# Kernel tuning notes

Measured on AMD Instinct MI355X. Metric: run time of the kernel, lower is better.

The kernel has to match this reference:

```python
import jax, jax.numpy as jnp
import numpy as np

N, IN_F, E, EDGE_F, H, C = 50000, 128, 800000, 32, 4, 32
NEG_SLOPE = 0.2
EPS = 1e-16


def setup_inputs() -> dict:
    key = jax.random.key(0)
    ks = jax.random.split(key, 10)
    s = lambda *sh: 1.0 / np.sqrt(sh[-1])
    return {
        "node_features": jax.random.normal(ks[0], (N, IN_F), jnp.float32),
        "edge_features": jax.random.normal(ks[1], (E, EDGE_F), jnp.float32),
        "edge_index": jax.random.randint(ks[2], (2, E), 0, N, jnp.int32),
        # GATConv params
        "W_gat": jax.random.normal(ks[3], (H * C, IN_F), jnp.float32) * s(IN_F),
        "att_src": jax.random.normal(ks[4], (H, C), jnp.float32) * s(C),
        "att_dst": jax.random.normal(ks[5], (H, C), jnp.float32) * s(C),
        "att_edge": jax.random.normal(ks[6], (H, C), jnp.float32) * s(C),
        "bias": jnp.zeros((H * C,), jnp.float32),
        # edge_linear and skip_connection weights
        "W_edge": jax.random.normal(ks[7], (H * C, EDGE_F), jnp.float32) * s(EDGE_F),
        "W_skip": jax.random.normal(ks[8], (H * C, IN_F), jnp.float32) * s(IN_F),
    }


def reference(node_features, edge_features, edge_index, W_gat, att_src, att_dst,
              att_edge, bias, W_edge, W_skip):
    src, dst = edge_index[0], edge_index[1]
    # edge_linear + view(-1, H, C)
    e_attr = (edge_features @ W_edge.T).reshape(E, H, C)
    # GATConv: per-head linear transform of nodes -> [N, H, C]
    x = (node_features @ W_gat.T).reshape(N, H, C)
    # attention logits: a_src.x_i + a_dst.x_j + a_edge.e  -> [E, H]
    a_src = jnp.einsum('nhc,hc->nh', x, att_src)
    a_dst = jnp.einsum('nhc,hc->nh', x, att_dst)
    a_edge = jnp.einsum('ehc,hc->eh', e_attr, att_edge)
    alpha = jax.nn.leaky_relu(a_src[src] + a_dst[dst] + a_edge, NEG_SLOPE)
    # segment softmax over incoming edges of each destination node
    m = jax.ops.segment_max(alpha, dst, num_segments=N)  # [N, H]
    m = jnp.where(jnp.isfinite(m), m, 0.0)
    ex = jnp.exp(alpha - m[dst])
    denom = jax.ops.segment_sum(ex, dst, num_segments=N)  # [N, H]
    attn = ex / (denom[dst] + EPS)  # [E, H]
    # message = alpha * x_src ; scatter-add to destination
    msg = x[src] * attn[:, :, None]  # [E, H, C]
    out = jax.ops.segment_sum(msg, dst, num_segments=N)  # [N, H, C]
    out = out.reshape(N, H * C) + bias  # concat=True
    # skip connection + ELU activation
    out = out + node_features @ W_skip.T
    return jax.nn.elu(out)
```

## Files before the change

### kernel.cpp

```cpp
#include <hip/hip_runtime.h>
#include <hip/hip_bf16.h>

constexpr int N_NODES = 50000;
constexpr int IN_F    = 128;
constexpr long E_EDGES = 800000;
constexpr int EDGE_F  = 32;
constexpr int H_HEADS = 4;
constexpr int C_CH    = 32;
constexpr int HC      = 128;
constexpr float NEG_SLOPE = 0.2f;
constexpr float EPS = 1e-16f;
constexpr int NB_SCAN = (N_NODES + 255) / 256;
constexpr int NB_HIST = (int)((E_EDGES + 255) / 256);
constexpr float SM_SHIFT = 12.0f;

typedef __attribute__((ext_vector_type(8))) short bf16x8;
typedef __attribute__((ext_vector_type(4))) float f32x4;

__device__ __forceinline__ unsigned short f2b(float f) {
    __hip_bfloat16 h = __float2bfloat16(f);
    return *reinterpret_cast<unsigned short*>(&h);
}
__device__ __forceinline__ float b2f_lo(unsigned v) { return __uint_as_float(v << 16); }
__device__ __forceinline__ float b2f_hi(unsigned v) { return __uint_as_float(v & 0xffff0000u); }

__global__ __launch_bounds__(256) void prep_kernel(
    const float* __restrict__ Wg, const float* __restrict__ Ws,
    unsigned short* __restrict__ wcat, const float* __restrict__ We,
    const float* __restrict__ att_edge, float* __restrict__ weff,
    const int* __restrict__ dst, int* __restrict__ counts,
    int* __restrict__ rank)
{
    const int b = blockIdx.x, t = threadIdx.x;
    if (b < 32) {
        int i = (b * 256 + t) * 4;
        const float* srcp = (i < 16384) ? (Wg + i) : (Ws + i - 16384);
        float4 v = *(const float4*)srcp;
        ushort4 o;
        o.x = f2b(v.x); o.y = f2b(v.y); o.z = f2b(v.z); o.w = f2b(v.w);
        *(ushort4*)&wcat[i] = o;
    } else if (b == 32) {
        if (t < 128) {
            int h = t >> 5, f = t & 31;
            float acc = 0.f;
#pragma unroll
            for (int c = 0; c < C_CH; ++c)
                acc = fmaf(We[(h * C_CH + c) * EDGE_F + f], att_edge[h * C_CH + c], acc);
            weff[t] = acc;
        }
    } else {
        long e = (long)(b - 33) * 256 + t;
        if (e < E_EDGES) rank[e] = atomicAdd(&counts[dst[e]], 1);
    }
}

__global__ __launch_bounds__(256) void mfma_gemm_kernel(
    const float* __restrict__ nf, const unsigned short* __restrict__ wcat,
    const float* __restrict__ bias, unsigned short* __restrict__ xb,
    float* __restrict__ out)
{
    const int t  = threadIdx.x;
    const int w  = t >> 6;
    const int l  = t & 63;
    const int lr = l & 15;
    const int lk = l >> 4;
    const int n0 = blockIdx.x * 64;

    bf16x8 bfr[4][4];
#pragma unroll
    for (int nfr = 0; nfr < 4; ++nfr)
#pragma unroll
        for (int ks = 0; ks < 4; ++ks)
            bfr[nfr][ks] = *(const bf16x8*)&wcat[(w * 64 + nfr * 16 + lr) * 128 + ks * 32 + lk * 8];

    f32x4 acc[4][4];
#pragma unroll
    for (int mf = 0; mf < 4; ++mf)
#pragma unroll
        for (int nfr = 0; nfr < 4; ++nfr)
            acc[mf][nfr] = (f32x4){0.f, 0.f, 0.f, 0.f};

#pragma unroll
    for (int ks = 0; ks < 4; ++ks) {
        bf16x8 afr[4];
#pragma unroll
        for (int mf = 0; mf < 4; ++mf) {
            int row = n0 + mf * 16 + lr;
            row = row < N_NODES ? row : N_NODES - 1;
            const float* ap = nf + (size_t)row * IN_F + ks * 32 + lk * 8;
            float4 a0 = *(const float4*)ap;
            float4 a1 = *(const float4*)(ap + 4);
            bf16x8 f;
            f[0] = (short)f2b(a0.x); f[1] = (short)f2b(a0.y);
            f[2] = (short)f2b(a0.z); f[3] = (short)f2b(a0.w);
            f[4] = (short)f2b(a1.x); f[5] = (short)f2b(a1.y);
            f[6] = (short)f2b(a1.z); f[7] = (short)f2b(a1.w);
            afr[mf] = f;
        }
#pragma unroll
        for (int mf = 0; mf < 4; ++mf)
#pragma unroll
            for (int nfr = 0; nfr < 4; ++nfr)
                acc[mf][nfr] = __builtin_amdgcn_mfma_f32_16x16x32_bf16(
                    afr[mf], bfr[nfr][ks], acc[mf][nfr], 0, 0, 0);
    }

#pragma unroll
    for (int nfr = 0; nfr < 4; ++nfr) {
        const int gc = w * 64 + nfr * 16 + lr;
        if (gc < HC) {
#pragma unroll
            for (int mf = 0; mf < 4; ++mf)
#pragma unroll
                for (int r = 0; r < 4; ++r) {
                    int m = n0 + mf * 16 + lk * 4 + r;
                    if (m < N_NODES) xb[(size_t)m * HC + gc] = f2b(acc[mf][nfr][r]);
                }
        } else {
            const float bv = bias[gc - HC];
#pragma unroll
            for (int mf = 0; mf < 4; ++mf)
#pragma unroll
                for (int r = 0; r < 4; ++r) {
                    int m = n0 + mf * 16 + lk * 4 + r;
                    if (m < N_NODES) out[(size_t)m * HC + gc - HC] = acc[mf][nfr][r] + bv;
                }
        }
    }
}

__global__ __launch_bounds__(256) void a_kernel(
    const unsigned int* __restrict__ xb32, const float* __restrict__ att_src,
    const float* __restrict__ att_dst, float* __restrict__ asrc,
    float* __restrict__ adst)
{
    const int wave = threadIdx.x >> 6, lane = threadIdx.x & 63;
    const int n = blockIdx.x * 4 + wave;
    if (n >= N_NODES) return;
    unsigned v = xb32[(size_t)n * 64 + lane];
    float x0 = b2f_lo(v), x1 = b2f_hi(v);
    float2 as = ((const float2*)att_src)[lane];
    float2 ad = ((const float2*)att_dst)[lane];
    float ps = x0 * as.x + x1 * as.y;
    float pd = x0 * ad.x + x1 * ad.y;
#pragma unroll
    for (int off = 1; off < 16; off <<= 1) {
        ps += __shfl_xor(ps, off);
        pd += __shfl_xor(pd, off);
    }
    if ((lane & 15) == 0) {
        asrc[(size_t)n * H_HEADS + (lane >> 4)] = ps;
        adst[(size_t)n * H_HEADS + (lane >> 4)] = pd;
    }
}

__global__ __launch_bounds__(256) void scan1_kernel(const int* __restrict__ counts,
                                                    int* __restrict__ row_ptr,
                                                    int* __restrict__ blocksum)
{
    __shared__ int s[256];
    int t = threadIdx.x;
    int i = blockIdx.x * 256 + t;
    int v = (i < N_NODES) ? counts[i] : 0;
    s[t] = v;
    __syncthreads();
#pragma unroll
    for (int off = 1; off < 256; off <<= 1) {
        int u = (t >= off) ? s[t - off] : 0;
        __syncthreads();
        s[t] += u;
        __syncthreads();
    }
    if (i < N_NODES) row_ptr[i] = s[t] - v;
    if (t == 255) blocksum[blockIdx.x] = s[255];
}

__global__ __launch_bounds__(256) void scan2_kernel(int* __restrict__ blocksum)
{
    __shared__ int s[256];
    int t = threadIdx.x;
    int v = (t < NB_SCAN) ? blocksum[t] : 0;
    s[t] = v;
    __syncthreads();
#pragma unroll
    for (int off = 1; off < 256; off <<= 1) {
        int u = (t >= off) ? s[t - off] : 0;
        __syncthreads();
        s[t] += u;
        __syncthreads();
    }
    blocksum[t] = s[t] - v;
}

__global__ __launch_bounds__(256) void scan3_kernel(int* __restrict__ row_ptr,
                                                    const int* __restrict__ blocksum)
{
    int i = blockIdx.x * 256 + threadIdx.x;
    if (i < N_NODES) row_ptr[i] = row_ptr[i] + blocksum[blockIdx.x];
    if (i == 0) row_ptr[N_NODES] = (int)E_EDGES;
}

__global__ __launch_bounds__(256) void edge_logits_kernel(
    const float* __restrict__ ef, const int* __restrict__ src,
    const int* __restrict__ dst, const float* __restrict__ weff,
    const float* __restrict__ asrc, const float* __restrict__ adst,
    const int* __restrict__ row_ptr, const int* __restrict__ rank,
    unsigned int* __restrict__ rec)
{
    __shared__ float ef_lds[64][36];
    __shared__ float wf[4][36];
    const int t = threadIdx.x;
    const long e0 = (long)blockIdx.x * 64;

#pragma unroll
    for (int j = 0; j < 2; ++j) {
        int i4 = t + j * 256;
        int el = i4 >> 3, f4 = i4 & 7;
        long e = e0 + el;
        float4 v = (e < E_EDGES) ? ((const float4*)ef)[e * 8 + f4]
                                 : make_float4(0.f, 0.f, 0.f, 0.f);
        ef_lds[el][f4 * 4 + 0] = v.x; ef_lds[el][f4 * 4 + 1] = v.y;
        ef_lds[el][f4 * 4 + 2] = v.z; ef_lds[el][f4 * 4 + 3] = v.w;
    }
    if (t < 128) wf[t >> 5][t & 31] = weff[t];
    __syncthreads();

    const int el = t >> 2, h = t & 3;
    const long e = e0 + el;
    if (e < E_EDGES) {
        float acc = 0.f;
#pragma unroll
        for (int f4 = 0; f4 < 8; ++f4) {
            float4 a = *(const float4*)&ef_lds[el][f4 * 4];
            float4 b = *(const float4*)&wf[h][f4 * 4];
            acc = fmaf(a.x, b.x, acc); acc = fmaf(a.y, b.y, acc);
            acc = fmaf(a.z, b.z, acc); acc = fmaf(a.w, b.w, acc);
        }
        int s = src[e], d = dst[e];
        float logit = asrc[(size_t)s * H_HEADS + h] + adst[(size_t)d * H_HEADS + h] + acc;
        float al = logit > 0.f ? logit : NEG_SLOPE * logit;
        int pos = row_ptr[d] + rank[e];
        unsigned w = (__float_as_uint(al) & 0xFFFFFF00u)
                   | ((unsigned)(s >> (8 * h)) & 0xFFu);
        rec[(size_t)pos * 4 + h] = w;
    }
}

__device__ __forceinline__ void accum8(float* acc, uint4 v, float e) {
    acc[0] = fmaf(b2f_lo(v.x), e, acc[0]);
    acc[1] = fmaf(b2f_hi(v.x), e, acc[1]);
    acc[2] = fmaf(b2f_lo(v.y), e, acc[2]);
    acc[3] = fmaf(b2f_hi(v.y), e, acc[3]);
    acc[4] = fmaf(b2f_lo(v.z), e, acc[4]);
    acc[5] = fmaf(b2f_hi(v.z), e, acc[5]);
    acc[6] = fmaf(b2f_lo(v.w), e, acc[6]);
    acc[7] = fmaf(b2f_hi(v.w), e, acc[7]);
}

__device__ __forceinline__ int rec_src(uint4 r) {
    return (int)((r.x & 0xFFu) | ((r.y & 0xFFu) << 8));
}
__device__ __forceinline__ float rec_alpha(uint4 r, int h) {
    unsigned w = h == 0 ? r.x : h == 1 ? r.y : h == 2 ? r.z : r.w;
    return __uint_as_float(w & 0xFFFFFF00u);
}

__global__ __launch_bounds__(256) void aggregate_kernel(
    const int* __restrict__ row_ptr, const uint4* __restrict__ rec4,
    const uint4* __restrict__ xb4, float* __restrict__ out)
{
    const int wave = threadIdx.x >> 6;
    const int lane = threadIdx.x & 63;
    const int d = blockIdx.x * 4 + wave;
    if (d >= N_NODES) return;
    const int beg = row_ptr[d], end = row_ptr[d + 1];
    const int q  = lane >> 4;
    const int cg = lane & 15;
    const int h  = cg >> 2;

    float acc[8] = {0.f, 0.f, 0.f, 0.f, 0.f, 0.f, 0.f, 0.f};
    float dsum = 0.f;

    int i = beg;
    for (; i + 8 <= end; i += 8) {
        int i0 = i + q, i1 = i + 4 + q;
        uint4 r0 = rec4[i0];
        uint4 r1 = rec4[i1];
        int s0 = rec_src(r0);
        int s1 = rec_src(r1);
        float a0 = rec_alpha(r0, h);
        float a1 = rec_alpha(r1, h);
        uint4 v0 = xb4[(size_t)s0 * 16 + cg];
        uint4 v1 = xb4[(size_t)s1 * 16 + cg];
        float e0 = __expf(a0 - SM_SHIFT);
        float e1 = __expf(a1 - SM_SHIFT);
        dsum += e0 + e1;
        accum8(acc, v0, e0);
        accum8(acc, v1, e1);
    }
    for (; i < end; i += 4) {
        int idx = i + q;
        bool val = idx < end;
        int ii = val ? idx : end - 1;
        uint4 r = rec4[ii];
        int s = rec_src(r);
        float a = rec_alpha(r, h);
        uint4 v = xb4[(size_t)s * 16 + cg];
        float e = val ? __expf(a - SM_SHIFT) : 0.f;
        dsum += e;
        accum8(acc, v, e);
    }

#pragma unroll
    for (int off = 16; off <= 32; off <<= 1) {
        dsum += __shfl_xor(dsum, off);
#pragma unroll
        for (int k = 0; k < 8; ++k) acc[k] += __shfl_xor(acc[k], off);
    }
    const float inv = 1.f / (dsum + EPS);

    if (q == 0) {
        float* op = out + (size_t)d * HC + cg * 8;
        float4 o0 = *(const float4*)op;
        float4 o1 = *(const float4*)(op + 4);
        o0.x += acc[0] * inv; o0.y += acc[1] * inv;
        o0.z += acc[2] * inv; o0.w += acc[3] * inv;
        o1.x += acc[4] * inv; o1.y += acc[5] * inv;
        o1.z += acc[6] * inv; o1.w += acc[7] * inv;
        o0.x = o0.x > 0.f ? o0.x : expf(o0.x) - 1.f;
        o0.y = o0.y > 0.f ? o0.y : expf(o0.y) - 1.f;
        o0.z = o0.z > 0.f ? o0.z : expf(o0.z) - 1.f;
        o0.w = o0.w > 0.f ? o0.w : expf(o0.w) - 1.f;
        o1.x = o1.x > 0.f ? o1.x : expf(o1.x) - 1.f;
        o1.y = o1.y > 0.f ? o1.y : expf(o1.y) - 1.f;
        o1.z = o1.z > 0.f ? o1.z : expf(o1.z) - 1.f;
        o1.w = o1.w > 0.f ? o1.w : expf(o1.w) - 1.f;
        *(float4*)op = o0;
        *(float4*)(op + 4) = o1;
    }
}

extern "C" void kernel_launch(void* const* d_in, const int* in_sizes, int n_in,
                              void* d_out, int out_size, void* d_ws, size_t ws_size,
                              hipStream_t stream)
{
    const float* nf       = (const float*)d_in[0];
    const float* ef       = (const float*)d_in[1];
    const int*   ei       = (const int*)d_in[2];
    const float* Wg       = (const float*)d_in[3];
    const float* att_src  = (const float*)d_in[4];
    const float* att_dst  = (const float*)d_in[5];
    const float* att_edge = (const float*)d_in[6];
    const float* bias     = (const float*)d_in[7];
    const float* We       = (const float*)d_in[8];
    const float* Ws       = (const float*)d_in[9];
    float* out = (float*)d_out;

    const int* src = ei;
    const int* dst = ei + E_EDGES;

    unsigned int* rec   = (unsigned int*)d_ws;
    unsigned short* xb  = (unsigned short*)(rec + 4 * E_EDGES);
    unsigned short* wcat= xb + (size_t)N_NODES * HC;
    float* asrc         = (float*)(wcat + 256 * 128);
    float* adst         = asrc + (size_t)N_NODES * H_HEADS;
    float* weff         = adst + (size_t)N_NODES * H_HEADS;
    int*   counts       = (int*)(weff + 128);
    int*   row_ptr      = counts + N_NODES;
    int*   blocksum     = row_ptr + N_NODES + 1;
    int*   rank         = blocksum + 256;

    (void)hipMemsetAsync(counts, 0, (size_t)N_NODES * sizeof(int), stream);

    prep_kernel<<<33 + NB_HIST, 256, 0, stream>>>(
        Wg, Ws, wcat, We, att_edge, weff, dst, counts, rank);
    mfma_gemm_kernel<<<(N_NODES + 63) / 64, 256, 0, stream>>>(
        nf, wcat, bias, xb, out);
    a_kernel<<<(N_NODES + 3) / 4, 256, 0, stream>>>(
        (const unsigned int*)xb, att_src, att_dst, asrc, adst);
    scan1_kernel<<<NB_SCAN, 256, 0, stream>>>(counts, row_ptr, blocksum);
    scan2_kernel<<<1, 256, 0, stream>>>(blocksum);
    scan3_kernel<<<NB_SCAN, 256, 0, stream>>>(row_ptr, blocksum);
    edge_logits_kernel<<<(int)(E_EDGES / 64), 256, 0, stream>>>(
        ef, src, dst, weff, asrc, adst, row_ptr, rank, rec);
    aggregate_kernel<<<(N_NODES + 3) / 4, 256, 0, stream>>>(
        row_ptr, (const uint4*)rec, (const uint4*)xb, out);
}
```

Baseline: 175.5 us.

## Split edge logit computation into streaming kernel plus separate CSR scatter

Edge logits are now computed one thread per edge with all four heads in registers and written as a contiguous uint4 in edge order. A separate kernel then scatters each 16-byte record into CSR position using row_ptr and rank. Previously each head wrote 4 bytes to a scattered position. The split also removes the LDS staging of edge features. In exchange it adds an extra 12.8MB intermediate buffer write plus read and one more kernel launch.

New measurement: 190.0 us. 1.08x slower.

```diff
diff --git a/kernel.cpp b/kernel.cpp
--- a/kernel.cpp
+++ b/kernel.cpp
@@ -200,49 +200,59 @@
     if (i == 0) row_ptr[N_NODES] = (int)E_EDGES;
 }
 
-__global__ __launch_bounds__(256) void edge_logits_kernel(
+__global__ __launch_bounds__(256) void el_stream_kernel(
     const float* __restrict__ ef, const int* __restrict__ src,
     const int* __restrict__ dst, const float* __restrict__ weff,
     const float* __restrict__ asrc, const float* __restrict__ adst,
-    const int* __restrict__ row_ptr, const int* __restrict__ rank,
-    unsigned int* __restrict__ rec)
-{
-    __shared__ float ef_lds[64][36];
-    __shared__ float wf[4][36];
+    uint4* __restrict__ rec_e)
+{
+    __shared__ float wf[128];
     const int t = threadIdx.x;
-    const long e0 = (long)blockIdx.x * 64;
-
-#pragma unroll
-    for (int j = 0; j < 2; ++j) {
-        int i4 = t + j * 256;
-        int el = i4 >> 3, f4 = i4 & 7;
-        long e = e0 + el;
-        float4 v = (e < E_EDGES) ? ((const float4*)ef)[e * 8 + f4]
-                                 : make_float4(0.f, 0.f, 0.f, 0.f);
-        ef_lds[el][f4 * 4 + 0] = v.x; ef_lds[el][f4 * 4 + 1] = v.y;
-        ef_lds[el][f4 * 4 + 2] = v.z; ef_lds[el][f4 * 4 + 3] = v.w;
-    }
-    if (t < 128) wf[t >> 5][t & 31] = weff[t];
+    if (t < 128) wf[t] = weff[t];
     __syncthreads();
 
-    const int el = t >> 2, h = t & 3;
-    const long e = e0 + el;
+    const long e = (long)blockIdx.x * 256 + t;
+    if (e >= E_EDGES) return;
+
+    const float4* ef4 = (const float4*)ef;
+    float4 q[8];
+#pragma unroll
+    for (int j = 0; j < 8; ++j) q[j] = ef4[(size_t)e * 8 + j];
+
+    const int s = src[e], d = dst[e];
+    float4 as4 = ((const float4*)asrc)[s];
+    float4 ad4 = ((const float4*)adst)[d];
+    float base[4] = {as4.x + ad4.x, as4.y + ad4.y, as4.z + ad4.z, as4.w + ad4.w};
+
+    uint4 r;
+    unsigned* rw = (unsigned*)&r;
+#pragma unroll
+    for (int h = 0; h < 4; ++h) {
+        float acc = 0.f;
+#pragma unroll
+        for (int f4 = 0; f4 < 8; ++f4) {
+            float4 w4 = *(const float4*)&wf[h * 32 + f4 * 4];
+            acc = fmaf(q[f4].x, w4.x, acc); acc = fmaf(q[f4].y, w4.y, acc);
+            acc = fmaf(q[f4].z, w4.z, acc); acc = fmaf(q[f4].w, w4.w, acc);
+        }
+        float logit = base[h] + acc;
+        float al = logit > 0.f ? logit : NEG_SLOPE * logit;
+        rw[h] = (__float_as_uint(al) & 0xFFFFFF00u)
+              | ((unsigned)(s >> (8 * h)) & 0xFFu);
+    }
+    rec_e[e] = r;
+}
+
+__global__ __launch_bounds__(256) void scatter_kernel(
+    const int* __restrict__ dst, const int* __restrict__ rank,
+    const int* __restrict__ row_ptr, const uint4* __restrict__ rec_e,
+    uint4* __restrict__ rec_s)
+{
+    const long e = (long)blockIdx.x * 256 + threadIdx.x;
     if (e < E_EDGES) {
-        float acc = 0.f;
-#pragma unroll
-        for (int f4 = 0; f4 < 8; ++f4) {
-            float4 a = *(const float4*)&ef_lds[el][f4 * 4];
-            float4 b = *(const float4*)&wf[h][f4 * 4];
-            acc = fmaf(a.x, b.x, acc); acc = fmaf(a.y, b.y, acc);
-            acc = fmaf(a.z, b.z, acc); acc = fmaf(a.w, b.w, acc);
-        }
-        int s = src[e], d = dst[e];
-        float logit = asrc[(size_t)s * H_HEADS + h] + adst[(size_t)d * H_HEADS + h] + acc;
-        float al = logit > 0.f ? logit : NEG_SLOPE * logit;
+        int d = dst[e];
         int pos = row_ptr[d] + rank[e];
-        unsigned w = (__float_as_uint(al) & 0xFFFFFF00u)
-                   | ((unsigned)(s >> (8 * h)) & 0xFFu);
-        rec[(size_t)pos * 4 + h] = w;
+        rec_s[pos] = rec_e[e];
     }
 }
 
@@ -359,8 +369,9 @@
     const int* src = ei;
     const int* dst = ei + E_EDGES;
 
-    unsigned int* rec   = (unsigned int*)d_ws;
-    unsigned short* xb  = (unsigned short*)(rec + 4 * E_EDGES);
+    unsigned int* rec_s = (unsigned int*)d_ws;
+    unsigned int* rec_e = rec_s + 4 * E_EDGES;
+    unsigned short* xb  = (unsigned short*)(rec_e + 4 * E_EDGES);
     unsigned short* wcat= xb + (size_t)N_NODES * HC;
     float* asrc         = (float*)(wcat + 256 * 128);
     float* adst         = asrc + (size_t)N_NODES * H_HEADS;
@@ -381,8 +392,10 @@
     scan1_kernel<<<NB_SCAN, 256, 0, stream>>>(counts, row_ptr, blocksum);
     scan2_kernel<<<1, 256, 0, stream>>>(blocksum);
     scan3_kernel<<<NB_SCAN, 256, 0, stream>>>(row_ptr, blocksum);
-    edge_logits_kernel<<<(int)(E_EDGES / 64), 256, 0, stream>>>(
-        ef, src, dst, weff, asrc, adst, row_ptr, rank, rec);
+    el_stream_kernel<<<NB_HIST, 256, 0, stream>>>(
+        ef, src, dst, weff, asrc, adst, (uint4*)rec_e);
+    scatter_kernel<<<NB_HIST, 256, 0, stream>>>(
+        dst, rank, row_ptr, (const uint4*)rec_e, (uint4*)rec_s);
     aggregate_kernel<<<(N_NODES + 3) / 4, 256, 0, stream>>>(
-        row_ptr, (const uint4*)rec, (const uint4*)xb, out);
-}
+        row_ptr, (const uint4*)rec_s, (const uint4*)xb, out);
+}
```
